# Performance work log

Measured on AMD Instinct MI355X. Metric: run time of the kernel, lower is better.

Reference implementation:

```python
import jax, jax.numpy as jnp
import numpy as np

N, E, F_IN, HID, HEADS, OUT, EDIM = 50000, 800000, 128, 64, 2, 40, 5
NEG_SLOPE = 0.2


def setup_inputs() -> dict:
    key = jax.random.key(0)
    ks = jax.random.split(key, 16)
    x = jax.random.normal(ks[0], (N, F_IN), jnp.float32)
    # build edge_index with src != dst so PyG's remove_self_loops is a no-op
    dst = jax.random.randint(ks[1], (E,), 0, N, dtype=jnp.int32)
    off = jax.random.randint(ks[2], (E,), 1, N, dtype=jnp.int32)
    src = (dst + off) % N
    edge_index = jnp.stack([src, dst], axis=0)
    edge_attr = jax.random.normal(ks[3], (E, EDIM), jnp.float32)
    s = 0.1
    params = dict(
        W1=jax.random.normal(ks[4], (F_IN, HEADS * HID), jnp.float32) * s,
        att_src1=jax.random.normal(ks[5], (HEADS, HID), jnp.float32) * s,
        att_dst1=jax.random.normal(ks[6], (HEADS, HID), jnp.float32) * s,
        We1=jax.random.normal(ks[7], (EDIM, HEADS * HID), jnp.float32) * s,
        att_e1=jax.random.normal(ks[8], (HEADS, HID), jnp.float32) * s,
        b1=jnp.zeros((HEADS * HID,), jnp.float32),
        W2=jax.random.normal(ks[9], (HEADS * HID, OUT), jnp.float32) * s,
        att_src2=jax.random.normal(ks[10], (1, OUT), jnp.float32) * s,
        att_dst2=jax.random.normal(ks[11], (1, OUT), jnp.float32) * s,
        We2=jax.random.normal(ks[12], (EDIM, OUT), jnp.float32) * s,
        att_e2=jax.random.normal(ks[13], (1, OUT), jnp.float32) * s,
        b2=jnp.zeros((OUT,), jnp.float32),
    )
    return dict(x=x, edge_index=edge_index, edge_attr=edge_attr, **params)


def _add_self_loops(src, dst, eattr, n):
    # PyG add_self_loops with fill_value='mean': per-dst-node mean of incoming edge_attr
    cnt = jax.ops.segment_sum(jnp.ones_like(dst, jnp.float32), dst, num_segments=n)
    loop_attr = jax.ops.segment_sum(eattr, dst, num_segments=n) / jnp.maximum(cnt, 1.0)[:, None]
    ar = jnp.arange(n, dtype=src.dtype)
    return (jnp.concatenate([src, ar]), jnp.concatenate([dst, ar]),
            jnp.concatenate([eattr, loop_attr], axis=0))


def _gat_conv(x, src, dst, eattr, W, a_src, a_dst, We, a_e, b):
    n = x.shape[0]
    H, C = a_src.shape
    xh = (x @ W).reshape(n, H, C)                      # [N,H,C]
    al_src = jnp.einsum('nhc,hc->nh', xh, a_src)[src]  # [Etot,H]
    al_dst = jnp.einsum('nhc,hc->nh', xh, a_dst)[dst]
    eh = (eattr @ We).reshape(-1, H, C)                # [Etot,H,C]
    al_e = jnp.einsum('ehc,hc->eh', eh, a_e)
    alpha = jax.nn.leaky_relu(al_src + al_dst + al_e, negative_slope=NEG_SLOPE)
    amax = jax.ops.segment_max(alpha, dst, num_segments=n)  # segment-wise softmax over dst
    ex = jnp.exp(alpha - amax[dst])
    denom = jax.ops.segment_sum(ex, dst, num_segments=n)
    alpha = ex / (denom[dst] + 1e-16)
    out = jax.ops.segment_sum(xh[src] * alpha[:, :, None], dst, num_segments=n)
    return out.reshape(n, H * C) + b


def reference(x, edge_index, edge_attr, W1, att_src1, att_dst1, We1, att_e1, b1,
              W2, att_src2, att_dst2, We2, att_e2, b2):
    src, dst = edge_index[0], edge_index[1]
    s2, d2, ea2 = _add_self_loops(src, dst, edge_attr, x.shape[0])
    h = jax.nn.elu(_gat_conv(x, s2, d2, ea2, W1, att_src1, att_dst1, We1, att_e1, b1))
    logits = _gat_conv(h, s2, d2, ea2, W2, att_src2, att_dst2, We2, att_e2, b2)
    return jax.nn.log_softmax(logits, axis=1)
```

## Files before the change

### kernel.cpp

```cpp
#include <hip/hip_runtime.h>
#include <hip/hip_fp16.h>
#include <math.h>

#define N_NODES 50000
#define N_EDGES 800000
#define F_IN    128
#define HID     64
#define HEADS   2
#define C1      128
#define OUT_C   40
#define EDIM    5
#define NEG_SLOPE 0.2f
#define CAPN    64
#define NPB1    16
#define NPB2    8
#define SCAN_B  256
#define SCAN_NB ((N_NODES + SCAN_B - 1) / SCAN_B)

typedef __bf16 bf16x8 __attribute__((ext_vector_type(8)));
typedef float  f32x4v __attribute__((ext_vector_type(4)));

constexpr size_t pad64(size_t n){ return (n + 63) / 64 * 64; }
constexpr size_t O_CNT      = 0;
constexpr size_t O_ZERO_END = O_CNT      + pad64(N_NODES);
constexpr size_t O_RANK     = O_ZERO_END;
constexpr size_t O_ROWPTR   = O_RANK     + pad64(N_EDGES);
constexpr size_t O_STMP     = O_ROWPTR   + pad64(N_NODES+1);
constexpr size_t O_BSUM     = O_STMP     + pad64(N_NODES);
constexpr size_t O_BOFF     = O_BSUM     + pad64(SCAN_NB);
constexpr size_t O_EREC     = O_BOFF     + pad64(SCAN_NB);
constexpr size_t O_WEATT    = O_EREC     + pad64((size_t)N_EDGES*2);
constexpr size_t O_XHB      = O_WEATT    + 64;
constexpr size_t O_AS1      = O_XHB      + pad64((size_t)N_NODES*C1/2);
constexpr size_t O_AD1      = O_AS1      + pad64((size_t)N_NODES*2);
constexpr size_t O_H1       = O_AD1      + pad64((size_t)N_NODES*2);
constexpr size_t O_XH2B     = O_H1       + pad64((size_t)N_NODES*C1);
constexpr size_t O_AS2      = O_XH2B     + pad64((size_t)N_NODES*OUT_C/2);
constexpr size_t O_AD2      = O_AS2      + pad64(N_NODES);

__device__ __forceinline__ float lrelu(float v){ return v >= 0.f ? v : NEG_SLOPE*v; }
__device__ __forceinline__ float bfl(unsigned u){ return __uint_as_float(u << 16); }
__device__ __forceinline__ float bfh(unsigned u){ return __uint_as_float(u & 0xFFFF0000u); }
__device__ __forceinline__ unsigned short f2bf(float f){
  unsigned u = __float_as_uint(f);
  return (unsigned short)((u + 0x7FFFu + ((u >> 16) & 1u)) >> 16);
}
__device__ __forceinline__ unsigned f2h(float f){
  return (unsigned)__half_as_ushort(__float2half(f));
}
__device__ __forceinline__ float h2f(unsigned u){
  return __half2float(__ushort_as_half((unsigned short)(u & 0xFFFFu)));
}

__global__ void k_count(const int* __restrict__ dst, int* __restrict__ cnt,
                        int* __restrict__ rank){
  int e = blockIdx.x*blockDim.x + threadIdx.x;
  if (e >= N_EDGES) return;
  rank[e] = atomicAdd(&cnt[dst[e]], 1);
}

__global__ void __launch_bounds__(SCAN_B) k_scan1(const int* __restrict__ cnt,
                                                  int* __restrict__ stmp,
                                                  int* __restrict__ bsum){
  int blk = blockIdx.x, t = threadIdx.x;
  int i = blk*SCAN_B + t;
  int v = (i < N_NODES) ? cnt[i] : 0;
  int lane = t & 63, w = t >> 6;
  int x = v;
  #pragma unroll
  for (int off = 1; off < 64; off <<= 1){
    int y = __shfl_up(x, off);
    if (lane >= off) x += y;
  }
  __shared__ int wsum[SCAN_B/64];
  if (lane == 63) wsum[w] = x;
  __syncthreads();
  int add = 0;
  for (int k = 0; k < w; k++) add += wsum[k];
  x += add;
  if (i < N_NODES) stmp[i] = x;
  if (t == SCAN_B-1) bsum[blk] = x;
}

__global__ void __launch_bounds__(SCAN_B) k_scan2(const int* __restrict__ bsum,
                                                  int* __restrict__ boff,
                                                  const float* __restrict__ We1,
                                                  const float* __restrict__ ae1,
                                                  const float* __restrict__ We2,
                                                  const float* __restrict__ ae2,
                                                  float* __restrict__ weatt){
  int t = threadIdx.x;
  int v = (t < SCAN_NB) ? bsum[t] : 0;
  int lane = t & 63, w = t >> 6;
  int x = v;
  #pragma unroll
  for (int off = 1; off < 64; off <<= 1){
    int y = __shfl_up(x, off);
    if (lane >= off) x += y;
  }
  __shared__ int wsum[SCAN_B/64];
  if (lane == 63) wsum[w] = x;
  __syncthreads();
  int add = 0;
  for (int k = 0; k < w; k++) add += wsum[k];
  x += add;
  if (t < SCAN_NB) boff[t] = x - v;
  if (t < 10){
    int k = t >> 1, h = t & 1;
    float s = 0.f;
    for (int c = 0; c < HID; c++) s += We1[k*C1 + h*HID + c] * ae1[h*HID + c];
    weatt[k*2 + h] = s;
  } else if (t < 15){
    int k = t - 10;
    float s = 0.f;
    for (int c = 0; c < OUT_C; c++) s += We2[k*OUT_C + c] * ae2[c];
    weatt[10 + k] = s;
  }
}

__global__ void __launch_bounds__(SCAN_B) k_scan3(const int* __restrict__ stmp,
                                                  const int* __restrict__ boff,
                                                  int* __restrict__ rowptr){
  int blk = blockIdx.x, t = threadIdx.x;
  int i = blk*SCAN_B + t;
  if (i < N_NODES) rowptr[i+1] = stmp[i] + boff[blk];
  if (i == 0) rowptr[0] = 0;
}

__global__ void k_scatter(const int* __restrict__ src, const int* __restrict__ dst,
                          const int* __restrict__ rank,
                          const float* __restrict__ eattr, const int* __restrict__ rowptr,
                          const float* __restrict__ weatt,
                          uint2* __restrict__ erec){
  int e = blockIdx.x*blockDim.x + threadIdx.x;
  if (e >= N_EDGES) return;
  int d = dst[e];
  int pos = rowptr[d] + rank[e];
  float a[EDIM];
  #pragma unroll
  for (int k = 0; k < EDIM; k++) a[k] = eattr[e*EDIM + k];
  float l0 = 0.f, l1 = 0.f, l2 = 0.f;
  #pragma unroll
  for (int k = 0; k < EDIM; k++){
    l0 += a[k]*weatt[k*2 + 0];
    l1 += a[k]*weatt[k*2 + 1];
    l2 += a[k]*weatt[10 + k];
  }
  unsigned w0 = (unsigned)src[e] | (f2h(l2) << 16);
  unsigned w1 = f2h(l0) | (f2h(l1) << 16);
  erec[pos] = make_uint2(w0, w1);
}

__global__ void __launch_bounds__(256) k_gemm1(const float* __restrict__ x,
                                               const float* __restrict__ W,
                                               const float* __restrict__ a_src,
                                               const float* __restrict__ a_dst,
                                               unsigned short* __restrict__ xhb,
                                               float* __restrict__ as_o,
                                               float* __restrict__ ad_o){
  __shared__ __align__(16) unsigned char smem[128*136*2];
  __bf16 (*wt)[136] = (__bf16(*)[136])smem;
  float  (*eps)[132] = (float(*)[132])smem;
  int tid = threadIdx.x;
  int wv = tid >> 6, L = tid & 63;
  int g = L >> 4, c16 = L & 15;
  int r0 = blockIdx.x * 64;

  for (int i = tid; i < F_IN*C1; i += 256){
    int k = i >> 7, c = i & 127;
    wt[c][k] = (__bf16)W[i];
  }
  __syncthreads();

  f32x4v acc[8];
  #pragma unroll
  for (int ct = 0; ct < 8; ct++) acc[ct] = (f32x4v){0.f, 0.f, 0.f, 0.f};

  int arow = r0 + wv*16 + c16;
  bool aok = arow < N_NODES;
  const float* xrow = &x[(size_t)arow*F_IN];
  #pragma unroll
  for (int ks = 0; ks < 4; ks++){
    int k0 = ks*32 + g*8;
    bf16x8 a;
    if (aok){
      float4 v0 = *(const float4*)&xrow[k0];
      float4 v1 = *(const float4*)&xrow[k0 + 4];
      a[0]=(__bf16)v0.x; a[1]=(__bf16)v0.y; a[2]=(__bf16)v0.z; a[3]=(__bf16)v0.w;
      a[4]=(__bf16)v1.x; a[5]=(__bf16)v1.y; a[6]=(__bf16)v1.z; a[7]=(__bf16)v1.w;
    } else {
      a = (bf16x8)(__bf16)0.f;
    }
    #pragma unroll
    for (int ct = 0; ct < 8; ct++){
      bf16x8 b = *(const bf16x8*)&wt[ct*16 + c16][k0];
      acc[ct] = __builtin_amdgcn_mfma_f32_16x16x32_bf16(a, b, acc[ct], 0, 0, 0);
    }
  }
  __syncthreads();

  #pragma unroll
  for (int ct = 0; ct < 8; ct++){
    #pragma unroll
    for (int r = 0; r < 4; r++)
      eps[wv*16 + g*4 + r][ct*16 + c16] = acc[ct][r];
  }
  __syncthreads();

  int row = tid >> 2, cb = tid & 3;
  int grow = r0 + row;
  float vals[32];
  #pragma unroll
  for (int j = 0; j < 32; j++) vals[j] = eps[row][cb*32 + j];
  if (grow < N_NODES){
    unsigned pk[16];
    #pragma unroll
    for (int j = 0; j < 16; j++)
      pk[j] = (unsigned)f2bf(vals[2*j]) | ((unsigned)f2bf(vals[2*j+1]) << 16);
    uint4* d4 = (uint4*)&xhb[(size_t)grow*C1 + cb*32];
    d4[0] = make_uint4(pk[0],pk[1],pk[2],pk[3]);
    d4[1] = make_uint4(pk[4],pk[5],pk[6],pk[7]);
    d4[2] = make_uint4(pk[8],pk[9],pk[10],pk[11]);
    d4[3] = make_uint4(pk[12],pk[13],pk[14],pk[15]);
  }
  float s = 0.f, d = 0.f;
  #pragma unroll
  for (int j = 0; j < 32; j++){
    s += vals[j]*a_src[cb*32 + j];
    d += vals[j]*a_dst[cb*32 + j];
  }
  s += __shfl_xor(s, 1);
  d += __shfl_xor(d, 1);
  if ((cb & 1) == 0 && grow < N_NODES){
    int h = cb >> 1;
    as_o[grow*2 + h] = s;
    ad_o[grow*2 + h] = d;
  }
}

__global__ void __launch_bounds__(256) k_agg1(const unsigned short* __restrict__ xhb,
    const int* __restrict__ rowptr, const uint2* __restrict__ erec,
    const float* __restrict__ as1, const float* __restrict__ ad1,
    const float* __restrict__ b1, float* __restrict__ h1){
  __shared__ float2 eC[NPB1][CAPN+1];
  __shared__ int    sC[NPB1][CAPN+1];
  int t = threadIdx.x;
  int g = t >> 4, l = t & 15;
  int n = blockIdx.x*NPB1 + g;
  if (n >= N_NODES) return;
  int beg = rowptr[n], end = rowptr[n+1];
  int deg = end - beg;
  float2 adn = *(const float2*)&ad1[n*2];
  bool cached = (deg <= CAPN);

  float s0 = 0.f, s1 = 0.f, la0 = 0.f, la1 = 0.f;
  for (int i = l; i < deg; i += 16){
    uint2 r = erec[(size_t)beg + i];
    int s = r.x & 0xFFFFu;
    float al0 = h2f(r.y), al1 = h2f(r.y >> 16);
    float2 a = *(const float2*)&as1[s*2];
    float e0 = expf(lrelu(a.x + adn.x + al0));
    float e1 = expf(lrelu(a.y + adn.y + al1));
    if (cached){ sC[g][i] = s * C1; eC[g][i] = make_float2(e0, e1); }
    s0 += e0; s1 += e1; la0 += al0; la1 += al1;
  }
  #pragma unroll
  for (int off = 1; off < 16; off <<= 1){
    s0 += __shfl_xor(s0, off); s1 += __shfl_xor(s1, off);
    la0 += __shfl_xor(la0, off); la1 += __shfl_xor(la1, off);
  }
  float inv = 1.f / fmaxf((float)deg, 1.f);
  float2 asn = *(const float2*)&as1[n*2];
  float sl0 = lrelu(asn.x + adn.x + la0*inv);
  float sl1 = lrelu(asn.y + adn.y + la1*inv);
  float es0 = expf(sl0), es1 = expf(sl1);
  float S0 = s0 + es0 + 1e-16f;
  float S1 = s1 + es1 + 1e-16f;

  int head = l >> 3;
  float acc[8];
  #pragma unroll
  for (int j = 0; j < 8; j++) acc[j] = 0.f;
  if (cached){
    for (int k = 0; k < deg; k++){
      float2 e2 = eC[g][k];
      float e = head ? e2.y : e2.x;
      uint4 r = *(const uint4*)&xhb[sC[g][k] + l*8];
      acc[0] += e*bfl(r.x); acc[1] += e*bfh(r.x);
      acc[2] += e*bfl(r.y); acc[3] += e*bfh(r.y);
      acc[4] += e*bfl(r.z); acc[5] += e*bfh(r.z);
      acc[6] += e*bfl(r.w); acc[7] += e*bfh(r.w);
    }
  } else {
    for (int k = 0; k < deg; k++){
      uint2 rr = erec[(size_t)beg + k];
      int s = rr.x & 0xFFFFu;
      float2 a = *(const float2*)&as1[s*2];
      float e = head ? expf(lrelu(a.y + adn.y + h2f(rr.y >> 16)))
                     : expf(lrelu(a.x + adn.x + h2f(rr.y)));
      uint4 r = *(const uint4*)&xhb[(size_t)s*C1 + l*8];
      acc[0] += e*bfl(r.x); acc[1] += e*bfh(r.x);
      acc[2] += e*bfl(r.y); acc[3] += e*bfh(r.y);
      acc[4] += e*bfl(r.z); acc[5] += e*bfh(r.z);
      acc[6] += e*bfl(r.w); acc[7] += e*bfh(r.w);
    }
  }
  float es = head ? es1 : es0;
  float den = head ? S1 : S0;
  uint4 r = *(const uint4*)&xhb[(size_t)n*C1 + l*8];
  float xs8[8];
  xs8[0]=bfl(r.x); xs8[1]=bfh(r.x); xs8[2]=bfl(r.y); xs8[3]=bfh(r.y);
  xs8[4]=bfl(r.z); xs8[5]=bfh(r.z); xs8[6]=bfl(r.w); xs8[7]=bfh(r.w);
  float o[8];
  #pragma unroll
  for (int j = 0; j < 8; j++){
    float v = (acc[j] + es*xs8[j]) / den + b1[l*8 + j];
    o[j] = v > 0.f ? v : expm1f(v);
  }
  *(float4*)&h1[(size_t)n*C1 + l*8]     = make_float4(o[0],o[1],o[2],o[3]);
  *(float4*)&h1[(size_t)n*C1 + l*8 + 4] = make_float4(o[4],o[5],o[6],o[7]);
}

#define T2_ROWS 128
#define T2_KK   32
__global__ void __launch_bounds__(256) k_gemm2(const float* __restrict__ h1,
    const float* __restrict__ W2, const float* __restrict__ a_src2,
    const float* __restrict__ a_dst2,
    unsigned short* __restrict__ xh2b, float* __restrict__ as_o, float* __restrict__ ad_o){
  __shared__ float hs[T2_ROWS][T2_KK+1];
  __shared__ float ws[F_IN*OUT_C];
  int tid = threadIdx.x;
  int tx = tid & 7, ty = tid >> 3;
  int r0 = blockIdx.x * T2_ROWS;
  for (int i = tid; i < F_IN*OUT_C/4; i += 256)
    ((float4*)ws)[i] = ((const float4*)W2)[i];
  float acc[4][5];
  #pragma unroll
  for (int i = 0; i < 4; i++)
    #pragma unroll
    for (int j = 0; j < 5; j++) acc[i][j] = 0.f;

  for (int kb = 0; kb < F_IN; kb += T2_KK){
    __syncthreads();
    for (int i = tid; i < T2_ROWS*(T2_KK/4); i += 256){
      int r = i >> 3, c4 = (i & 7) * 4;
      int row = r0 + r;
      float4 v = (row < N_NODES) ? *(const float4*)&h1[(size_t)row*F_IN + kb + c4]
                                 : make_float4(0.f,0.f,0.f,0.f);
      hs[r][c4+0]=v.x; hs[r][c4+1]=v.y; hs[r][c4+2]=v.z; hs[r][c4+3]=v.w;
    }
    __syncthreads();
    #pragma unroll 4
    for (int k = 0; k < T2_KK; k++){
      float a[4], b[5];
      #pragma unroll
      for (int i = 0; i < 4; i++) a[i] = hs[ty*4 + i][k];
      #pragma unroll
      for (int j = 0; j < 5; j++) b[j] = ws[(kb + k)*OUT_C + tx*5 + j];
      #pragma unroll
      for (int i = 0; i < 4; i++)
        #pragma unroll
        for (int j = 0; j < 5; j++)
          acc[i][j] += a[i]*b[j];
    }
  }
  float asv[5], adv[5];
  #pragma unroll
  for (int j = 0; j < 5; j++){
    asv[j] = a_src2[tx*5 + j];
    adv[j] = a_dst2[tx*5 + j];
  }
  #pragma unroll
  for (int i = 0; i < 4; i++){
    int row = r0 + ty*4 + i;
    bool ok = row < N_NODES;
    if (ok){
      #pragma unroll
      for (int j = 0; j < 5; j++)
        xh2b[(size_t)row*OUT_C + tx*5 + j] = f2bf(acc[i][j]);
    }
    float s = 0.f, d = 0.f;
    #pragma unroll
    for (int j = 0; j < 5; j++){ s += acc[i][j]*asv[j]; d += acc[i][j]*adv[j]; }
    s += __shfl_xor(s, 1); s += __shfl_xor(s, 2); s += __shfl_xor(s, 4);
    d += __shfl_xor(d, 1); d += __shfl_xor(d, 2); d += __shfl_xor(d, 4);
    if (ok && tx == 0){
      as_o[row] = s;
      ad_o[row] = d;
    }
  }
}

__global__ void __launch_bounds__(256) k_agg2(const unsigned short* __restrict__ xh2b,
    const int* __restrict__ rowptr, const uint2* __restrict__ erec,
    const float* __restrict__ as2, const float* __restrict__ ad2,
    const float* __restrict__ b2, float* __restrict__ out){
  __shared__ float eC[NPB2][CAPN+1];
  __shared__ int   sC[NPB2][CAPN+1];
  int t = threadIdx.x;
  int g = t >> 5, l = t & 31;
  int n = blockIdx.x*NPB2 + g;
  if (n >= N_NODES) return;
  int beg = rowptr[n], end = rowptr[n+1];
  int deg = end - beg;
  float adv = ad2[n];
  bool cached = (deg <= CAPN);

  float ss = 0.f, la = 0.f;
  for (int i = l; i < deg; i += 32){
    uint2 r = erec[(size_t)beg + i];
    int s = r.x & 0xFFFFu;
    float al2 = h2f(r.x >> 16);
    float e = expf(lrelu(as2[s] + adv + al2));
    if (cached){ sC[g][i] = s * OUT_C; eC[g][i] = e; }
    ss += e; la += al2;
  }
  #pragma unroll
  for (int off = 1; off < 32; off <<= 1){
    ss += __shfl_xor(ss, off);
    la += __shfl_xor(la, off);
  }
  float inv = 1.f / fmaxf((float)deg, 1.f);
  float sl = lrelu(as2[n] + adv + la*inv);
  float es = expf(sl);
  float S = ss + es + 1e-16f;

  float a0 = 0.f, a1 = 0.f;
  if (l < 20){
    if (cached){
      for (int k = 0; k < deg; k++){
        float e = eC[g][k];
        unsigned u = *(const unsigned*)&xh2b[sC[g][k] + l*2];
        a0 += e*bfl(u); a1 += e*bfh(u);
      }
    } else {
      for (int k = 0; k < deg; k++){
        uint2 rr = erec[(size_t)beg + k];
        int s = rr.x & 0xFFFFu;
        float e = expf(lrelu(as2[s] + adv + h2f(rr.x >> 16)));
        unsigned u = *(const unsigned*)&xh2b[(size_t)s*OUT_C + l*2];
        a0 += e*bfl(u); a1 += e*bfh(u);
      }
    }
  }
  float o0 = -INFINITY, o1 = -INFINITY;
  if (l < 20){
    unsigned u = *(const unsigned*)&xh2b[(size_t)n*OUT_C + l*2];
    o0 = (a0 + es*bfl(u)) / S + b2[l*2 + 0];
    o1 = (a1 + es*bfh(u)) / S + b2[l*2 + 1];
  }
  float mm = fmaxf(o0, o1);
  #pragma unroll
  for (int off = 1; off < 32; off <<= 1) mm = fmaxf(mm, __shfl_xor(mm, off));
  float e = (l < 20) ? (expf(o0 - mm) + expf(o1 - mm)) : 0.f;
  #pragma unroll
  for (int off = 1; off < 32; off <<= 1) e += __shfl_xor(e, off);
  if (l < 20){
    float lse = logf(e);
    out[(size_t)n*OUT_C + l*2 + 0] = o0 - mm - lse;
    out[(size_t)n*OUT_C + l*2 + 1] = o1 - mm - lse;
  }
}

extern "C" void kernel_launch(void* const* d_in, const int* in_sizes, int n_in,
                              void* d_out, int out_size, void* d_ws, size_t ws_size,
                              hipStream_t stream){
  const float* x        = (const float*)d_in[0];
  const int*   ei       = (const int*)  d_in[1];
  const float* eattr    = (const float*)d_in[2];
  const float* W1       = (const float*)d_in[3];
  const float* att_src1 = (const float*)d_in[4];
  const float* att_dst1 = (const float*)d_in[5];
  const float* We1      = (const float*)d_in[6];
  const float* att_e1   = (const float*)d_in[7];
  const float* b1       = (const float*)d_in[8];
  const float* W2       = (const float*)d_in[9];
  const float* att_src2 = (const float*)d_in[10];
  const float* att_dst2 = (const float*)d_in[11];
  const float* We2      = (const float*)d_in[12];
  const float* att_e2   = (const float*)d_in[13];
  const float* b2       = (const float*)d_in[14];
  const int* src = ei;
  const int* dst = ei + N_EDGES;

  float* wsf    = (float*)d_ws;
  int*   cnt     = (int*)(wsf + O_CNT);
  int*   rank    = (int*)(wsf + O_RANK);
  int*   rowptr  = (int*)(wsf + O_ROWPTR);
  int*   stmp    = (int*)(wsf + O_STMP);
  int*   bsum    = (int*)(wsf + O_BSUM);
  int*   boff    = (int*)(wsf + O_BOFF);
  uint2* erec    = (uint2*)(wsf + O_EREC);
  float* weatt   = wsf + O_WEATT;
  unsigned short* xhb  = (unsigned short*)(wsf + O_XHB);
  float* as1     = wsf + O_AS1;
  float* ad1     = wsf + O_AD1;
  float* h1      = wsf + O_H1;
  unsigned short* xh2b = (unsigned short*)(wsf + O_XH2B);
  float* as2     = wsf + O_AS2;
  float* ad2     = wsf + O_AD2;
  float* out     = (float*)d_out;

  hipMemsetAsync(wsf + O_CNT, 0, O_ZERO_END*sizeof(float), stream);

  const int EB = (N_EDGES + 255) / 256;

  k_count  <<<EB, 256, 0, stream>>>(dst, cnt, rank);
  k_scan1  <<<SCAN_NB, SCAN_B, 0, stream>>>(cnt, stmp, bsum);
  k_scan2  <<<1, SCAN_B, 0, stream>>>(bsum, boff, We1, att_e1, We2, att_e2, weatt);
  k_scan3  <<<SCAN_NB, SCAN_B, 0, stream>>>(stmp, boff, rowptr);
  k_scatter<<<EB, 256, 0, stream>>>(src, dst, rank, eattr, rowptr, weatt, erec);

  k_gemm1  <<<(N_NODES + 63)/64, 256, 0, stream>>>(x, W1, att_src1, att_dst1, xhb, as1, ad1);
  k_agg1   <<<(N_NODES + NPB1 - 1)/NPB1, 256, 0, stream>>>(xhb, rowptr, erec, as1, ad1, b1, h1);

  k_gemm2  <<<(N_NODES + T2_ROWS - 1)/T2_ROWS, 256, 0, stream>>>(h1, W2, att_src2, att_dst2,
                                                                 xh2b, as2, ad2);
  k_agg2   <<<(N_NODES + NPB2 - 1)/NPB2, 256, 0, stream>>>(xh2b, rowptr, erec, as2, ad2, b2, out);
}
```

Measured before the change: 179.1 us.

## Store layer-1 output as bf16 and use MFMA for second GEMM

```diff
diff --git a/kernel.cpp b/kernel.cpp
--- a/kernel.cpp
+++ b/kernel.cpp
@@ -33,8 +33,8 @@
 constexpr size_t O_XHB      = O_WEATT    + 64;
 constexpr size_t O_AS1      = O_XHB      + pad64((size_t)N_NODES*C1/2);
 constexpr size_t O_AD1      = O_AS1      + pad64((size_t)N_NODES*2);
-constexpr size_t O_H1       = O_AD1      + pad64((size_t)N_NODES*2);
-constexpr size_t O_XH2B     = O_H1       + pad64((size_t)N_NODES*C1);
+constexpr size_t O_H1B      = O_AD1      + pad64((size_t)N_NODES*2);
+constexpr size_t O_XH2B     = O_H1B      + pad64((size_t)N_NODES*C1/2);
 constexpr size_t O_AS2      = O_XH2B     + pad64((size_t)N_NODES*OUT_C/2);
 constexpr size_t O_AD2      = O_AS2      + pad64(N_NODES);
 
@@ -241,7 +241,7 @@
 __global__ void __launch_bounds__(256) k_agg1(const unsigned short* __restrict__ xhb,
     const int* __restrict__ rowptr, const uint2* __restrict__ erec,
     const float* __restrict__ as1, const float* __restrict__ ad1,
-    const float* __restrict__ b1, float* __restrict__ h1){
+    const float* __restrict__ b1, unsigned short* __restrict__ h1b){
   __shared__ float2 eC[NPB1][CAPN+1];
   __shared__ int    sC[NPB1][CAPN+1];
   int t = threadIdx.x;
@@ -311,83 +311,91 @@
   float xs8[8];
   xs8[0]=bfl(r.x); xs8[1]=bfh(r.x); xs8[2]=bfl(r.y); xs8[3]=bfh(r.y);
   xs8[4]=bfl(r.z); xs8[5]=bfh(r.z); xs8[6]=bfl(r.w); xs8[7]=bfh(r.w);
-  float o[8];
-  #pragma unroll
-  for (int j = 0; j < 8; j++){
-    float v = (acc[j] + es*xs8[j]) / den + b1[l*8 + j];
-    o[j] = v > 0.f ? v : expm1f(v);
-  }
-  *(float4*)&h1[(size_t)n*C1 + l*8]     = make_float4(o[0],o[1],o[2],o[3]);
-  *(float4*)&h1[(size_t)n*C1 + l*8 + 4] = make_float4(o[4],o[5],o[6],o[7]);
-}
-
-#define T2_ROWS 128
-#define T2_KK   32
-__global__ void __launch_bounds__(256) k_gemm2(const float* __restrict__ h1,
+  unsigned pk[4];
+  #pragma unroll
+  for (int p = 0; p < 4; p++){
+    float v0 = (acc[2*p]   + es*xs8[2*p])   / den + b1[l*8 + 2*p];
+    float v1 = (acc[2*p+1] + es*xs8[2*p+1]) / den + b1[l*8 + 2*p+1];
+    v0 = v0 > 0.f ? v0 : expm1f(v0);
+    v1 = v1 > 0.f ? v1 : expm1f(v1);
+    pk[p] = (unsigned)f2bf(v0) | ((unsigned)f2bf(v1) << 16);
+  }
+  *(uint4*)&h1b[(size_t)n*C1 + l*8] = make_uint4(pk[0], pk[1], pk[2], pk[3]);
+}
+
+__global__ void __launch_bounds__(256) k_gemm2(const unsigned short* __restrict__ h1b,
     const float* __restrict__ W2, const float* __restrict__ a_src2,
     const float* __restrict__ a_dst2,
     unsigned short* __restrict__ xh2b, float* __restrict__ as_o, float* __restrict__ ad_o){
-  __shared__ float hs[T2_ROWS][T2_KK+1];
-  __shared__ float ws[F_IN*OUT_C];
+  __shared__ __align__(16) unsigned char smem[64*52*4];
+  __bf16 (*wt)[136] = (__bf16(*)[136])smem;
+  float  (*eps)[52] = (float(*)[52])smem;
   int tid = threadIdx.x;
-  int tx = tid & 7, ty = tid >> 3;
-  int r0 = blockIdx.x * T2_ROWS;
-  for (int i = tid; i < F_IN*OUT_C/4; i += 256)
-    ((float4*)ws)[i] = ((const float4*)W2)[i];
-  float acc[4][5];
-  #pragma unroll
-  for (int i = 0; i < 4; i++)
+  int wv = tid >> 6, L = tid & 63;
+  int g = L >> 4, c16 = L & 15;
+  int r0 = blockIdx.x * 64;
+
+  for (int i = tid; i < 48*F_IN; i += 256){
+    int c = i >> 7, k = i & 127;
+    wt[c][k] = (c < OUT_C) ? (__bf16)W2[k*OUT_C + c] : (__bf16)0.f;
+  }
+  __syncthreads();
+
+  f32x4v acc[3];
+  #pragma unroll
+  for (int ct = 0; ct < 3; ct++) acc[ct] = (f32x4v){0.f, 0.f, 0.f, 0.f};
+
+  int arow = r0 + wv*16 + c16;
+  bool aok = arow < N_NODES;
+  const unsigned short* hrow = &h1b[(size_t)arow*C1];
+  #pragma unroll
+  for (int ks = 0; ks < 4; ks++){
+    int k0 = ks*32 + g*8;
+    bf16x8 a;
+    if (aok) a = *(const bf16x8*)&hrow[k0];
+    else     a = (bf16x8)(__bf16)0.f;
     #pragma unroll
-    for (int j = 0; j < 5; j++) acc[i][j] = 0.f;
-
-  for (int kb = 0; kb < F_IN; kb += T2_KK){
-    __syncthreads();
-    for (int i = tid; i < T2_ROWS*(T2_KK/4); i += 256){
-      int r = i >> 3, c4 = (i & 7) * 4;
-      int row = r0 + r;
-      float4 v = (row < N_NODES) ? *(const float4*)&h1[(size_t)row*F_IN + kb + c4]
-                                 : make_float4(0.f,0.f,0.f,0.f);
-      hs[r][c4+0]=v.x; hs[r][c4+1]=v.y; hs[r][c4+2]=v.z; hs[r][c4+3]=v.w;
-    }
-    __syncthreads();
-    #pragma unroll 4
-    for (int k = 0; k < T2_KK; k++){
-      float a[4], b[5];
-      #pragma unroll
-      for (int i = 0; i < 4; i++) a[i] = hs[ty*4 + i][k];
-      #pragma unroll
-      for (int j = 0; j < 5; j++) b[j] = ws[(kb + k)*OUT_C + tx*5 + j];
-      #pragma unroll
-      for (int i = 0; i < 4; i++)
-        #pragma unroll
-        for (int j = 0; j < 5; j++)
-          acc[i][j] += a[i]*b[j];
-    }
-  }
-  float asv[5], adv[5];
-  #pragma unroll
-  for (int j = 0; j < 5; j++){
-    asv[j] = a_src2[tx*5 + j];
-    adv[j] = a_dst2[tx*5 + j];
-  }
-  #pragma unroll
-  for (int i = 0; i < 4; i++){
-    int row = r0 + ty*4 + i;
-    bool ok = row < N_NODES;
-    if (ok){
-      #pragma unroll
-      for (int j = 0; j < 5; j++)
-        xh2b[(size_t)row*OUT_C + tx*5 + j] = f2bf(acc[i][j]);
-    }
-    float s = 0.f, d = 0.f;
+    for (int ct = 0; ct < 3; ct++){
+      bf16x8 b = *(const bf16x8*)&wt[ct*16 + c16][k0];
+      acc[ct] = __builtin_amdgcn_mfma_f32_16x16x32_bf16(a, b, acc[ct], 0, 0, 0);
+    }
+  }
+  __syncthreads();
+
+  #pragma unroll
+  for (int ct = 0; ct < 3; ct++){
     #pragma unroll
-    for (int j = 0; j < 5; j++){ s += acc[i][j]*asv[j]; d += acc[i][j]*adv[j]; }
-    s += __shfl_xor(s, 1); s += __shfl_xor(s, 2); s += __shfl_xor(s, 4);
-    d += __shfl_xor(d, 1); d += __shfl_xor(d, 2); d += __shfl_xor(d, 4);
-    if (ok && tx == 0){
-      as_o[row] = s;
-      ad_o[row] = d;
-    }
+    for (int r = 0; r < 4; r++)
+      eps[wv*16 + g*4 + r][ct*16 + c16] = acc[ct][r];
+  }
+  __syncthreads();
+
+  int row = tid >> 2, cb = tid & 3;
+  int grow = r0 + row;
+  int base = cb*12;
+  float vals[12];
+  #pragma unroll
+  for (int j = 0; j < 12; j++) vals[j] = eps[row][base + j];
+  int npair = (cb < 3) ? 6 : 2;
+  if (grow < N_NODES){
+    unsigned* dp = (unsigned*)&xh2b[(size_t)grow*OUT_C + base];
+    for (int jj = 0; jj < npair; jj++)
+      dp[jj] = (unsigned)f2bf(vals[2*jj]) | ((unsigned)f2bf(vals[2*jj+1]) << 16);
+  }
+  float s = 0.f, d = 0.f;
+  #pragma unroll
+  for (int j = 0; j < 12; j++){
+    int col = base + j;
+    if (col < OUT_C){
+      s += vals[j]*a_src2[col];
+      d += vals[j]*a_dst2[col];
+    }
+  }
+  s += __shfl_xor(s, 1); s += __shfl_xor(s, 2);
+  d += __shfl_xor(d, 1); d += __shfl_xor(d, 2);
+  if (cb == 0 && grow < N_NODES){
+    as_o[grow] = s;
+    ad_o[grow] = d;
   }
 }
 
@@ -495,7 +503,7 @@
   unsigned short* xhb  = (unsigned short*)(wsf + O_XHB);
   float* as1     = wsf + O_AS1;
   float* ad1     = wsf + O_AD1;
-  float* h1      = wsf + O_H1;
+  unsigned short* h1b  = (unsigned short*)(wsf + O_H1B);
   unsigned short* xh2b = (unsigned short*)(wsf + O_XH2B);
   float* as2     = wsf + O_AS2;
   float* ad2     = wsf + O_AD2;
@@ -512,9 +520,8 @@
   k_scatter<<<EB, 256, 0, stream>>>(src, dst, rank, eattr, rowptr, weatt, erec);
 
   k_gemm1  <<<(N_NODES + 63)/64, 256, 0, stream>>>(x, W1, att_src1, att_dst1, xhb, as1, ad1);
-  k_agg1   <<<(N_NODES + NPB1 - 1)/NPB1, 256, 0, stream>>>(xhb, rowptr, erec, as1, ad1, b1, h1);
-
-  k_gemm2  <<<(N_NODES + T2_ROWS - 1)/T2_ROWS, 256, 0, stream>>>(h1, W2, att_src2, att_dst2,
-                                                                 xh2b, as2, ad2);
+  k_agg1   <<<(N_NODES + NPB1 - 1)/NPB1, 256, 0, stream>>>(xhb, rowptr, erec, as1, ad1, b1, h1b);
+
+  k_gemm2  <<<(N_NODES + 63)/64, 256, 0, stream>>>(h1b, W2, att_src2, att_dst2, xh2b, as2, ad2);
   k_agg2   <<<(N_NODES + NPB2 - 1)/NPB2, 256, 0, stream>>>(xh2b, rowptr, erec, as2, ad2, b2, out);
 }
```

New measurement: 167.7 us. 1.07x faster.
